# Kernel optimization log

Measured on AMD Instinct MI355X. Metric: run time of the kernel, lower is better.

## Reference

```python
import jax, jax.numpy as jnp
import numpy as np

B, C0, N, K = 8, 3, 2048, 20
EMB = 1024
NUM_CLASS = 40
EPS = 1e-5
SLOPE = 0.2


def setup_inputs() -> dict:
    key = jax.random.key(0)
    ks = jax.random.split(key, 16)
    rn = lambda k, s: jax.random.normal(k, s, jnp.float32) * 0.05
    inp = {
        'x': jax.random.normal(ks[0], (B, C0, N), jnp.float32),
        # 1x1 conv weights (out_ch, in_ch)
        'w1': rn(ks[1], (64, 6)),
        'w2': rn(ks[2], (64, 128)),
        'w3': rn(ks[3], (128, 128)),
        'w4': rn(ks[4], (256, 256)),
        'w5': rn(ks[5], (EMB, 512)),
        # linear layers
        'lw1': rn(ks[6], (512, 2 * EMB)),
        'lw2': rn(ks[7], (256, 512)),
        'lb2': jnp.zeros((256,), jnp.float32),
        'lw3': rn(ks[8], (NUM_CLASS, 256)),
        'lb3': jnp.zeros((NUM_CLASS,), jnp.float32),
    }
    # batchnorm affine params (bn1..bn7)
    for i, c in zip(range(1, 8), (64, 64, 128, 256, EMB, 512, 256)):
        inp['g%d' % i] = jnp.ones((c,), jnp.float32)
        inp['b%d' % i] = jnp.zeros((c,), jnp.float32)
    return inp


def lrelu(x):
    return jnp.where(x >= 0, x, SLOPE * x)


def bn(x, g, b, axes):
    # training-mode batchnorm over `axes`, channel axis = 1 (or last for 2D)
    m = jnp.mean(x, axis=axes, keepdims=True)
    v = jnp.var(x, axis=axes, keepdims=True)
    shp = [1] * x.ndim
    ch_ax = 1 if x.ndim > 1 else 0
    shp[ch_ax] = g.shape[0]
    return (x - m) * jax.lax.rsqrt(v + EPS) * g.reshape(shp) + b.reshape(shp)


def knn_idx(x, k):
    # x: [B, C, N]; topk of -||xi - xj||^2 -> k nearest (incl. self)
    inner = -2.0 * jnp.einsum('bcn,bcm->bnm', x, x)
    xx = jnp.sum(x * x, axis=1)  # [B, N]
    pd = -xx[:, :, None] - inner - xx[:, None, :]
    return jax.lax.top_k(pd, k)[1]  # [B, N, k]


def graph_feature(x, k):
    # x: [B, C, N] -> [B, 2C, N, k]
    b_, c_, n_ = x.shape
    idx = knn_idx(x, k)
    xt = jnp.transpose(x, (0, 2, 1))  # [B, N, C]
    nbr = xt[jnp.arange(b_)[:, None, None], idx]  # [B, N, k, C] irregular gather
    ctr = xt[:, :, None, :]
    feat = jnp.concatenate([nbr - ctr, jnp.broadcast_to(ctr, nbr.shape)], axis=-1)
    return jnp.transpose(feat, (0, 3, 1, 2))


def edge_block(x, w, g, b, k):
    f = graph_feature(x, k)                      # [B, 2C, N, k]
    y = jnp.einsum('oc,bcnk->bonk', w, f)        # 1x1 conv2d
    y = lrelu(bn(y, g, b, (0, 2, 3)))
    return jnp.max(y, axis=-1)                   # max over k -> [B, O, N]


def reference(x, w1, w2, w3, w4, w5, lw1, lw2, lb2, lw3, lb3,
              g1, b1, g2, b2, g3, b3, g4, b4, g5, b5, g6, b6, g7, b7):
    x1 = edge_block(x, w1, g1, b1, K)   # [B, 64, N]
    x2 = edge_block(x1, w2, g2, b2, K)  # [B, 64, N]
    x3 = edge_block(x2, w3, g3, b3, K)  # [B, 128, N]
    x4 = edge_block(x3, w4, g4, b4, K)  # [B, 256, N]
    cat = jnp.concatenate([x1, x2, x3, x4], axis=1)  # [B, 512, N]
    y = lrelu(bn(jnp.einsum('oc,bcn->bon', w5, cat), g5, b5, (0, 2)))  # [B, EMB, N]
    p = jnp.concatenate([jnp.max(y, axis=-1), jnp.mean(y, axis=-1)], axis=1)  # [B, 2*EMB]
    h = lrelu(bn(p @ lw1.T, g6, b6, (0,)))
    h = lrelu(bn(h @ lw2.T + lb2, g7, b7, (0,)))  # dropout = identity (eval)
    return h @ lw3.T + lb3  # [B, NUM_CLASS]
```

## Files before the change

kernel.cpp:

```cpp
#include <hip/hip_runtime.h>
#include <float.h>

constexpr int cB = 8;
constexpr int cN = 2048;
constexpr int cKnn = 20;
constexpr float F_EPS = 1e-5f;
constexpr float F_SLOPE = 0.2f;

__device__ __forceinline__ float lrelu(float x){ return x >= 0.f ? x : F_SLOPE * x; }

typedef __bf16 bf16x8 __attribute__((ext_vector_type(8)));
typedef float  f32x4  __attribute__((ext_vector_type(4)));
union U16x8 { uint4 u; bf16x8 v; };

__device__ __forceinline__ unsigned short f2bf(float x){
    unsigned u = __builtin_bit_cast(unsigned, x);
    unsigned r = u + 0x7FFFu + ((u >> 16) & 1u);
    return (unsigned short)(r >> 16);
}
__device__ __forceinline__ float bf2f(unsigned short h){
    return __builtin_bit_cast(float, (unsigned)h << 16);
}
__device__ __forceinline__ bf16x8 ldfrag(const unsigned short* p){
    U16x8 t; t.u = *(const uint4*)p; return t.v;
}

__global__ void k_transpose3(const float* __restrict__ x, float* __restrict__ xt, float* __restrict__ xx){
    int i = blockIdx.x * 256 + threadIdx.x;
    if(i >= cB * cN) return;
    int b = i / cN, n = i % cN;
    const float* xb = x + (size_t)b * 3 * cN;
    float a = xb[n], c = xb[cN + n], d = xb[2*cN + n];
    float* o = xt + (size_t)i * 4;
    o[0] = a; o[1] = c; o[2] = d; o[3] = 0.f;
    xx[i] = a*a + c*c + d*d;
}

template<int C>
__global__ void k_xx(const float* __restrict__ xt, float* __restrict__ xx){
    int i = blockIdx.x * 256 + threadIdx.x;
    if(i >= cB * cN) return;
    const float4* r4 = (const float4*)(xt + (size_t)i * C);
    float s = 0.f;
    #pragma unroll
    for(int c = 0; c < C/4; c++){
        float4 v = r4[c];
        s += v.x*v.x + v.y*v.y + v.z*v.z + v.w*v.w;
    }
    xx[i] = s;
}

template<int C>
__global__ void k_mkhl(const float* __restrict__ xt, unsigned short* __restrict__ xhl){
    int i = blockIdx.x * 256 + threadIdx.x;
    if(i >= cB * cN * C) return;
    int c = i % C; size_t bn = (size_t)i / C;
    float x = xt[bn * C + c];
    unsigned short h = f2bf(x);
    unsigned short l = f2bf(x - bf2f(h));
    xhl[bn * 2 * C + c] = h;
    xhl[bn * 2 * C + C + c] = l;
}

template<int C>
__global__ __launch_bounds__(256) void k_score(const float* __restrict__ xt, const float* __restrict__ xx,
                                               float* __restrict__ S, int b_base){
    __shared__ float at[16][68];
    __shared__ float bt[16][68];
    int tid = threadIdx.x;
    int j0 = blockIdx.x * 64, q0 = blockIdx.y * 64, z = blockIdx.z;
    int b = b_base + z;
    const float* Xb = xt + (size_t)b * cN * C;
    int no = tid % 16, mo = tid / 16;
    float acc[4][4] = {};
    {
        if(tid < 64){
            float4 v = *(const float4*)(Xb + (size_t)(q0 + tid) * C);
            at[0][tid] = v.x; at[1][tid] = v.y; at[2][tid] = v.z; at[3][tid] = v.w;
            float4 w = *(const float4*)(Xb + (size_t)(j0 + tid) * C);
            bt[0][tid] = w.x; bt[1][tid] = w.y; bt[2][tid] = w.z; bt[3][tid] = w.w;
        }
        __syncthreads();
        #pragma unroll
        for(int c = 0; c < C; c++){
            float av[4] = { at[c][mo*4+0], at[c][mo*4+1], at[c][mo*4+2], at[c][mo*4+3] };
            float bv[4] = { bt[c][no*4+0], bt[c][no*4+1], bt[c][no*4+2], bt[c][no*4+3] };
            #pragma unroll
            for(int i2 = 0; i2 < 4; i2++)
                #pragma unroll
                for(int j2 = 0; j2 < 4; j2++)
                    acc[i2][j2] += av[i2] * bv[j2];
        }
    }
    const float* xxb = xx + (size_t)b * cN;
    float4 xv = *(const float4*)(xxb + j0 + no * 4);
    #pragma unroll
    for(int i2 = 0; i2 < 4; i2++){
        float4 o = make_float4(2.f*acc[i2][0] - xv.x, 2.f*acc[i2][1] - xv.y,
                               2.f*acc[i2][2] - xv.z, 2.f*acc[i2][3] - xv.w);
        *(float4*)(S + ((size_t)z * cN + q0 + mo * 4 + i2) * cN + j0 + no * 4) = o;
    }
}

template<int C>
__global__ __launch_bounds__(256) void k_score_mfma(const unsigned short* __restrict__ XHL,
                                                    const float* __restrict__ xx,
                                                    float* __restrict__ S, int b_base){
    constexpr int SROW = 2 * C;
    constexpr int KST = C / 32;
    __shared__ unsigned short As[128 * 40];
    __shared__ unsigned short Bs[128 * 40];
    int tid = threadIdx.x;
    int lane = tid & 63, wave = tid >> 6;
    int wm = wave & 1, wn = wave >> 1;
    int q0 = blockIdx.y * 128, j0 = blockIdx.x * 128, z = blockIdx.z;
    int b = b_base + z;
    const unsigned short* Xb = XHL + (size_t)b * cN * SROW;
    int m = lane & 15, quad = lane >> 4;
    f32x4 acc[4][4] = {};

    for(int seg = 0; seg < 3; seg++){
        int aoff = (seg == 2) ? C : 0;
        int boff = (seg == 1) ? C : 0;
        for(int kk = 0; kk < KST; kk++){
            __syncthreads();
            #pragma unroll
            for(int h = 0; h < 2; h++){
                int cidx = tid + h * 256;
                int row = cidx >> 2, cc = cidx & 3;
                *(uint4*)&As[row*40 + cc*8] = *(const uint4*)(Xb + (size_t)(q0 + row) * SROW + aoff + kk*32 + cc*8);
                *(uint4*)&Bs[row*40 + cc*8] = *(const uint4*)(Xb + (size_t)(j0 + row) * SROW + boff + kk*32 + cc*8);
            }
            __syncthreads();
            bf16x8 af[4], bfr[4];
            #pragma unroll
            for(int t = 0; t < 4; t++){
                af[t]  = ldfrag(&As[(wm*64 + t*16 + m)*40 + quad*8]);
                bfr[t] = ldfrag(&Bs[(wn*64 + t*16 + m)*40 + quad*8]);
            }
            #pragma unroll
            for(int i = 0; i < 4; i++)
                #pragma unroll
                for(int j = 0; j < 4; j++)
                    acc[i][j] = __builtin_amdgcn_mfma_f32_16x16x32_bf16(af[i], bfr[j], acc[i][j], 0, 0, 0);
        }
    }
    const float* xxb = xx + (size_t)b * cN;
    #pragma unroll
    for(int j = 0; j < 4; j++){
        int jj = j0 + wn*64 + j*16 + m;
        float xv = xxb[jj];
        #pragma unroll
        for(int i = 0; i < 4; i++){
            int r0 = q0 + wm*64 + i*16 + quad*4;
            #pragma unroll
            for(int r = 0; r < 4; r++)
                S[((size_t)z * cN + r0 + r) * cN + jj] = 2.f * acc[i][j][r] - xv;
        }
    }
}

__global__ __launch_bounds__(256) void k_select(const float* __restrict__ S, int* __restrict__ idxout,
                                                int b_base){
    __shared__ unsigned skey[2][44];
    __shared__ int      sidx[2][44];
    int tid = threadIdx.x;
    int wave = tid >> 6, lane = tid & 63;
    int row = wave >> 1;
    int w   = wave & 1;
    int n = blockIdx.x * 2 + row;
    int z = blockIdx.y;
    const float* rowp = S + ((size_t)z * cN + n) * cN + w * 1024;
    unsigned key[16];
    #pragma unroll
    for(int i = 0; i < 16; i++){
        float s = rowp[i * 64 + lane];
        unsigned u = __float_as_uint(s);
        key[i] = (s >= 0.f) ? (u | 0x80000000u) : ~u;
    }
    unsigned T = 0; bool exact = false;
    for(int bit = 31; bit >= 0; bit--){
        unsigned test = T | (1u << bit);
        int c = 0;
        #pragma unroll
        for(int i = 0; i < 16; i++) c += (key[i] >= test) ? 1 : 0;
        #pragma unroll
        for(int off = 32; off; off >>= 1) c += __shfl_xor(c, off);
        if(c >= cKnn){
            T = test;
            if(c == cKnn){ exact = true; break; }
        }
    }
    int jbase = w * 1024;
    int pos = 0;
    if(exact){
        #pragma unroll
        for(int i = 0; i < 16; i++){
            bool hi = key[i] >= T;
            unsigned long long mm = __ballot(hi);
            if(hi){
                int r = __popcll(mm & ((1ull << lane) - 1ull));
                skey[row][w*20 + pos + r] = key[i];
                sidx[row][w*20 + pos + r] = jbase + i*64 + lane;
            }
            pos += __popcll(mm);
        }
    } else {
        int nab = 0;
        #pragma unroll
        for(int i = 0; i < 16; i++) nab += (key[i] > T) ? 1 : 0;
        #pragma unroll
        for(int off = 32; off; off >>= 1) nab += __shfl_xor(nab, off);
        int need = cKnn - nab;
        #pragma unroll
        for(int i = 0; i < 16; i++){
            bool hi = key[i] > T;
            unsigned long long mm = __ballot(hi);
            if(hi){
                int r = __popcll(mm & ((1ull << lane) - 1ull));
                skey[row][w*20 + pos + r] = key[i];
                sidx[row][w*20 + pos + r] = jbase + i*64 + lane;
            }
            pos += __popcll(mm);
        }
        for(int i = 0; i < 16 && need > 0; i++){
            bool eq = (key[i] == T);
            unsigned long long mm = __ballot(eq);
            int r = __popcll(mm & ((1ull << lane) - 1ull));
            if(eq && r < need){
                skey[row][w*20 + pos + r] = key[i];
                sidx[row][w*20 + pos + r] = jbase + i*64 + lane;
            }
            int t = __popcll(mm); t = t < need ? t : need;
            pos += t; need -= t;
        }
    }
    __syncthreads();
    if(w) return;
    unsigned k40 = (lane < 40) ? skey[row][lane] : 0u;
    int      j40 = (lane < 40) ? sidx[row][lane] : 0;
    unsigned Tg = 0; bool ex = false;
    for(int bit = 31; bit >= 0; bit--){
        unsigned test = Tg | (1u << bit);
        int c = __popcll(__ballot((lane < 40) && (k40 >= test)));
        if(c >= cKnn){
            Tg = test;
            if(c == cKnn){ ex = true; break; }
        }
    }
    int* out = idxout + ((size_t)(b_base + z) * cN + n) * cKnn;
    if(ex){
        bool hi = (lane < 40) && (k40 >= Tg);
        unsigned long long mm = __ballot(hi);
        if(hi){ int r = __popcll(mm & ((1ull << lane) - 1ull)); out[r] = j40; }
    } else {
        bool hi = (lane < 40) && (k40 > Tg);
        unsigned long long mm = __ballot(hi);
        if(hi){ int r = __popcll(mm & ((1ull << lane) - 1ull)); out[r] = j40; }
        int nab = __popcll(mm);
        int need = cKnn - nab;
        bool eq = (lane < 40) && (k40 == Tg);
        unsigned long long me = __ballot(eq);
        int r = __popcll(me & ((1ull << lane) - 1ull));
        if(eq && r < need) out[nab + r] = j40;
    }
}

template<int Cin, int O, int CP>
__global__ void k_prepww(const float* __restrict__ w, float* __restrict__ ww){
    int e = blockIdx.x * 256 + threadIdx.x;
    if(e >= CP * 2 * O) return;
    int op = e % (2 * O), c = e / (2 * O);
    float val = 0.f;
    if(c < Cin){
        if(op < O) val = w[op * 2 * Cin + c];
        else { int o = op - O; val = w[o * 2 * Cin + Cin + c] - w[o * 2 * Cin + c]; }
    }
    ww[c * 2 * O + op] = val;
}

template<int Cin, int O, int CP>
__global__ void k_prepww_split(const float* __restrict__ w, unsigned short* __restrict__ whl){
    int e = blockIdx.x * 256 + threadIdx.x;
    if(e >= 2 * O * CP) return;
    int c = e % CP, o2 = e / CP;
    float val = 0.f;
    if(c < Cin){
        if(o2 < O) val = w[o2 * 2 * Cin + c];
        else { int o = o2 - O; val = w[o * 2 * Cin + Cin + c] - w[o * 2 * Cin + c]; }
    }
    unsigned short h = f2bf(val);
    unsigned short l = f2bf(val - bf2f(h));
    whl[(size_t)o2 * 2 * CP + c] = h;
    whl[(size_t)o2 * 2 * CP + CP + c] = l;
}

template<int K, int W2O>
__global__ __launch_bounds__(256) void k_uw(const float* __restrict__ xt, const float* __restrict__ ww,
                                            float* __restrict__ UW){
    __shared__ float at[16][68];
    __shared__ float bt[16][68];
    int tid = threadIdx.x;
    int o0 = blockIdx.x * 64, q0 = blockIdx.y * 64, b = blockIdx.z;
    const float* Xb = xt + (size_t)b * cN * K;
    int no = tid % 16, mo = tid / 16;
    float acc[4][4] = {};
    {
        if(tid < 64){
            float4 v = *(const float4*)(Xb + (size_t)(q0 + tid) * K);
            at[0][tid] = v.x; at[1][tid] = v.y; at[2][tid] = v.z; at[3][tid] = v.w;
            int cc = tid >> 4, n4 = tid & 15;
            float4 wv = *(const float4*)(ww + (size_t)cc * W2O + o0 + n4 * 4);
            bt[cc][n4*4+0] = wv.x; bt[cc][n4*4+1] = wv.y;
            bt[cc][n4*4+2] = wv.z; bt[cc][n4*4+3] = wv.w;
        }
        __syncthreads();
        #pragma unroll
        for(int c = 0; c < K; c++){
            float av[4] = { at[c][mo*4+0], at[c][mo*4+1], at[c][mo*4+2], at[c][mo*4+3] };
            float bv[4] = { bt[c][no*4+0], bt[c][no*4+1], bt[c][no*4+2], bt[c][no*4+3] };
            #pragma unroll
            for(int i2 = 0; i2 < 4; i2++)
                #pragma unroll
                for(int j2 = 0; j2 < 4; j2++)
                    acc[i2][j2] += av[i2] * bv[j2];
        }
    }
    #pragma unroll
    for(int i2 = 0; i2 < 4; i2++){
        float4 v = make_float4(acc[i2][0], acc[i2][1], acc[i2][2], acc[i2][3]);
        *(float4*)(UW + ((size_t)b * cN + q0 + mo * 4 + i2) * W2O + o0 + no * 4) = v;
    }
}

template<int C, int W2O>
__global__ __launch_bounds__(256) void k_uw_mfma(const unsigned short* __restrict__ XHL,
                                                 const unsigned short* __restrict__ WHL,
                                                 float* __restrict__ UW){
    constexpr int SROW = 2 * C;
    constexpr int KST = C / 32;
    __shared__ unsigned short As[128 * 40];
    __shared__ unsigned short Bs[128 * 40];
    int tid = threadIdx.x;
    int lane = tid & 63, wave = tid >> 6;
    int wm = wave & 1, wn = wave >> 1;
    int n0 = blockIdx.x * 128, q0 = blockIdx.y * 128, b = blockIdx.z;
    const unsigned short* Xb = XHL + (size_t)b * cN * SROW;
    int m = lane & 15, quad = lane >> 4;
    f32x4 acc[4][4] = {};

    for(int seg = 0; seg < 3; seg++){
        int aoff = (seg == 2) ? C : 0;
        int boff = (seg == 1) ? C : 0;
        for(int kk = 0; kk < KST; kk++){
            __syncthreads();
            #pragma unroll
            for(int h = 0; h < 2; h++){
                int cidx = tid + h * 256;
                int row = cidx >> 2, cc = cidx & 3;
                *(uint4*)&As[row*40 + cc*8] = *(const uint4*)(Xb + (size_t)(q0 + row) * SROW + aoff + kk*32 + cc*8);
                *(uint4*)&Bs[row*40 + cc*8] = *(const uint4*)(WHL + (size_t)(n0 + row) * SROW + boff + kk*32 + cc*8);
            }
            __syncthreads();
            bf16x8 af[4], bfr[4];
            #pragma unroll
            for(int t = 0; t < 4; t++){
                af[t]  = ldfrag(&As[(wm*64 + t*16 + m)*40 + quad*8]);
                bfr[t] = ldfrag(&Bs[(wn*64 + t*16 + m)*40 + quad*8]);
            }
            #pragma unroll
            for(int i = 0; i < 4; i++)
                #pragma unroll
                for(int j = 0; j < 4; j++)
                    acc[i][j] = __builtin_amdgcn_mfma_f32_16x16x32_bf16(af[i], bfr[j], acc[i][j], 0, 0, 0);
        }
    }
    #pragma unroll
    for(int i = 0; i < 4; i++){
        int r0 = q0 + wm*64 + i*16 + quad*4;
        #pragma unroll
        for(int j = 0; j < 4; j++){
            int col = n0 + wn*64 + j*16 + m;
            #pragma unroll
            for(int r = 0; r < 4; r++)
                UW[((size_t)b * cN + r0 + r) * W2O + col] = acc[i][j][r];
        }
    }
}

template<int O>
__global__ __launch_bounds__(256) void k_gmax(const float* __restrict__ UW, const int* __restrict__ idx,
                                              float* __restrict__ Mbuf, float* __restrict__ bsum, float* __restrict__ bsq){
    constexpr int VEC = O / 64;
    constexpr int W2O = 2 * O;
    int id = blockIdx.x;
    int b = id & 7;
    int base = (id >> 3) * 16;
    int tid = threadIdx.x;
    int w = tid >> 6, l = tid & 63;
    const float* U = UW + (size_t)b * cN * W2O;
    float lsum[VEC] = {}, lsq[VEC] = {};
    for(int p = 0; p < 4; p++){
        int n = base + w * 4 + p;
        const int* ip = idx + ((size_t)b * cN + n) * cKnn;
        int jj[cKnn];
        #pragma unroll
        for(int k = 0; k < cKnn; k++) jj[k] = ip[k];
        float mx[VEC], su[VEC] = {}, s2[VEC] = {};
        #pragma unroll
        for(int v = 0; v < VEC; v++) mx[v] = -FLT_MAX;
        #pragma unroll
        for(int k = 0; k < cKnn; k++){
            const float* ur = U + (size_t)jj[k] * W2O + l * VEC;
            float uv[VEC];
            if constexpr (VEC == 4){ float4 t = *(const float4*)ur; uv[0]=t.x; uv[1]=t.y; uv[2]=t.z; uv[3]=t.w; }
            else if constexpr (VEC == 2){ float2 t = *(const float2*)ur; uv[0]=t.x; uv[1]=t.y; }
            else { uv[0] = *ur; }
            #pragma unroll
            for(int v = 0; v < VEC; v++){
                mx[v] = fmaxf(mx[v], uv[v]); su[v] += uv[v]; s2[v] += uv[v]*uv[v];
            }
        }
        const float* wr = U + (size_t)n * W2O + O + l * VEC;
        float w2[VEC];
        if constexpr (VEC == 4){ float4 t = *(const float4*)wr; w2[0]=t.x; w2[1]=t.y; w2[2]=t.z; w2[3]=t.w; }
        else if constexpr (VEC == 2){ float2 t = *(const float2*)wr; w2[0]=t.x; w2[1]=t.y; }
        else { w2[0] = *wr; }
        float* mp = Mbuf + ((size_t)b * cN + n) * O + l * VEC;
        if constexpr (VEC == 4){
            *(float4*)mp = make_float4(mx[0]+w2[0], mx[1]+w2[1], mx[2]+w2[2], mx[3]+w2[3]);
        } else if constexpr (VEC == 2){
            *(float2*)mp = make_float2(mx[0]+w2[0], mx[1]+w2[1]);
        } else {
            *mp = mx[0] + w2[0];
        }
        #pragma unroll
        for(int v = 0; v < VEC; v++){
            lsum[v] += su[v] + (float)cKnn * w2[v];
            lsq[v]  += s2[v] + 2.f * w2[v] * su[v] + (float)cKnn * w2[v] * w2[v];
        }
    }
    int bkt = id & 63;
    #pragma unroll
    for(int v = 0; v < VEC; v++){
        atomicAdd(&bsum[bkt * O + l * VEC + v], lsum[v]);
        atomicAdd(&bsq [bkt * O + l * VEC + v], lsq[v]);
    }
}

template<int O>
__global__ void k_redstats(const float* __restrict__ bsum, const float* __restrict__ bsq,
                           const float* __restrict__ g, const float* __restrict__ bb,
                           float2* __restrict__ stats, float invcnt){
    int o = threadIdx.x;
    if(o >= O) return;
    float s = 0.f, q = 0.f;
    for(int k = 0; k < 64; k++){ s += bsum[k * O + o]; q += bsq[k * O + o]; }
    float m = s * invcnt;
    float v = q * invcnt - m * m;
    float sc = g[o] * rsqrtf(v + F_EPS);
    stats[o] = make_float2(sc, bb[o] - m * sc);
}

template<int O, bool WXT>
__global__ void k_norm(const float* __restrict__ Mbuf, const float2* __restrict__ stats,
                       unsigned short* __restrict__ catb, float* __restrict__ xtn, int ooff){
    size_t i = (size_t)blockIdx.x * 256 + threadIdx.x;
    if(i >= (size_t)cB * cN * O) return;
    int o = i % O;
    size_t bn = i / O;
    float2 st = stats[o];
    float y = lrelu(Mbuf[i] * st.x + st.y);
    catb[bn * 512 + ooff + o] = f2bf(y);
    if(WXT) xtn[i] = y;
}

__global__ void k_cvtw5(const float* __restrict__ w5, unsigned short* __restrict__ w5b){
    int i = blockIdx.x * 256 + threadIdx.x;
    if(i >= 1024 * 512) return;
    w5b[i] = f2bf(w5[i]);
}

__global__ __launch_bounds__(256) void k_gemm_z_mfma(const unsigned short* __restrict__ W5B,
                                                     const unsigned short* __restrict__ CATB,
                                                     float* __restrict__ z){
    __shared__ unsigned short As[128 * 40];
    __shared__ unsigned short Bs[128 * 40];
    int tid = threadIdx.x;
    int lane = tid & 63, wave = tid >> 6;
    int wm = wave & 1, wn = wave >> 1;
    int n0 = blockIdx.x * 128, o0 = blockIdx.y * 128, b = blockIdx.z;
    const unsigned short* Cb = CATB + (size_t)b * cN * 512;
    int m = lane & 15, quad = lane >> 4;
    f32x4 acc[4][4] = {};

    for(int kk = 0; kk < 16; kk++){
        __syncthreads();
        #pragma unroll
        for(int h = 0; h < 2; h++){
            int cidx = tid + h * 256;
            int row = cidx >> 2, cc = cidx & 3;
            *(uint4*)&As[row*40 + cc*8] = *(const uint4*)(W5B + (size_t)(o0 + row) * 512 + kk*32 + cc*8);
            *(uint4*)&Bs[row*40 + cc*8] = *(const uint4*)(Cb  + (size_t)(n0 + row) * 512 + kk*32 + cc*8);
        }
        __syncthreads();
        bf16x8 af[4], bfr[4];
        #pragma unroll
        for(int t = 0; t < 4; t++){
            af[t]  = ldfrag(&As[(wm*64 + t*16 + m)*40 + quad*8]);
            bfr[t] = ldfrag(&Bs[(wn*64 + t*16 + m)*40 + quad*8]);
        }
        #pragma unroll
        for(int i = 0; i < 4; i++)
            #pragma unroll
            for(int j = 0; j < 4; j++)
                acc[i][j] = __builtin_amdgcn_mfma_f32_16x16x32_bf16(af[i], bfr[j], acc[i][j], 0, 0, 0);
    }
    #pragma unroll
    for(int i = 0; i < 4; i++){
        int r0 = o0 + wm*64 + i*16 + quad*4;
        #pragma unroll
        for(int j = 0; j < 4; j++){
            int col = n0 + wn*64 + j*16 + m;
            #pragma unroll
            for(int r = 0; r < 4; r++)
                z[((size_t)b * 1024 + r0 + r) * cN + col] = acc[i][j][r];
        }
    }
}

__global__ void k_zstats(const float* __restrict__ z, const float* __restrict__ g5,
                         const float* __restrict__ b5, float2* __restrict__ stats){
    int o = blockIdx.x;
    int tid = threadIdx.x;
    __shared__ float ss[256], sq[256];
    float s = 0.f, q = 0.f;
    for(int e = tid; e < cB * cN; e += 256){
        int b = e >> 11, n = e & 2047;
        float v = z[((size_t)b * 1024 + o) * cN + n];
        s += v; q += v * v;
    }
    ss[tid] = s; sq[tid] = q; __syncthreads();
    for(int st = 128; st; st >>= 1){
        if(tid < st){ ss[tid] += ss[tid + st]; sq[tid] += sq[tid + st]; }
        __syncthreads();
    }
    if(tid == 0){
        float m = ss[0] / (float)(cB * cN);
        float v = sq[0] / (float)(cB * cN) - m * m;
        float sc = g5[o] * rsqrtf(v + F_EPS);
        stats[o] = make_float2(sc, b5[o] - m * sc);
    }
}

__global__ void k_pool(const float* __restrict__ z, const float2* __restrict__ stats,
                       float* __restrict__ p){
    int o = blockIdx.x, b = blockIdx.y;
    int tid = threadIdx.x;
    float2 st = stats[o];
    const float* row = z + ((size_t)b * 1024 + o) * cN;
    float mx = -FLT_MAX, sm = 0.f;
    for(int n = tid; n < cN; n += 256){
        float y = lrelu(row[n] * st.x + st.y);
        mx = fmaxf(mx, y); sm += y;
    }
    __shared__ float smx[256], ssm[256];
    smx[tid] = mx; ssm[tid] = sm; __syncthreads();
    for(int st2 = 128; st2; st2 >>= 1){
        if(tid < st2){ smx[tid] = fmaxf(smx[tid], smx[tid + st2]); ssm[tid] += ssm[tid + st2]; }
        __syncthreads();
    }
    if(tid == 0){
        p[(size_t)b * 2048 + o] = smx[0];
        p[(size_t)b * 2048 + 1024 + o] = ssm[0] * (1.f / cN);
    }
}

__global__ void k_fc1(const float* __restrict__ p, const float* __restrict__ lw1,
                      const float* __restrict__ g6, const float* __restrict__ b6,
                      float* __restrict__ h1){
    int f = blockIdx.x;
    int tid = threadIdx.x;
    const float* wrow = lw1 + (size_t)f * 2048;
    float acc[cB] = {};
    for(int i = tid; i < 2048; i += 64){
        float wv = wrow[i];
        #pragma unroll
        for(int b = 0; b < cB; b++) acc[b] += p[(size_t)b * 2048 + i] * wv;
    }
    #pragma unroll
    for(int b = 0; b < cB; b++){
        float v = acc[b];
        for(int off = 32; off; off >>= 1) v += __shfl_down(v, off);
        acc[b] = v;
    }
    if(tid == 0){
        float m = 0.f;
        #pragma unroll
        for(int b = 0; b < cB; b++) m += acc[b];
        m *= (1.f / cB);
        float var = 0.f;
        #pragma unroll
        for(int b = 0; b < cB; b++){ float d = acc[b] - m; var += d * d; }
        var *= (1.f / cB);
        float sc = g6[f] * rsqrtf(var + F_EPS);
        float sh = b6[f] - m * sc;
        #pragma unroll
        for(int b = 0; b < cB; b++) h1[(size_t)b * 512 + f] = lrelu(acc[b] * sc + sh);
    }
}

__global__ void k_fc2(const float* __restrict__ h1, const float* __restrict__ lw2,
                      const float* __restrict__ lb2, const float* __restrict__ g7,
                      const float* __restrict__ b7, float* __restrict__ h2){
    int f = blockIdx.x;
    int tid = threadIdx.x;
    const float* wrow = lw2 + (size_t)f * 512;
    float acc[cB] = {};
    for(int i = tid; i < 512; i += 64){
        float wv = wrow[i];
        #pragma unroll
        for(int b = 0; b < cB; b++) acc[b] += h1[(size_t)b * 512 + i] * wv;
    }
    #pragma unroll
    for(int b = 0; b < cB; b++){
        float v = acc[b];
        for(int off = 32; off; off >>= 1) v += __shfl_down(v, off);
        acc[b] = v;
    }
    if(tid == 0){
        float bias = lb2[f];
        #pragma unroll
        for(int b = 0; b < cB; b++) acc[b] += bias;
        float m = 0.f;
        #pragma unroll
        for(int b = 0; b < cB; b++) m += acc[b];
        m *= (1.f / cB);
        float var = 0.f;
        #pragma unroll
        for(int b = 0; b < cB; b++){ float d = acc[b] - m; var += d * d; }
        var *= (1.f / cB);
        float sc = g7[f] * rsqrtf(var + F_EPS);
        float sh = b7[f] - m * sc;
        #pragma unroll
        for(int b = 0; b < cB; b++) h2[(size_t)b * 256 + f] = lrelu(acc[b] * sc + sh);
    }
}

__global__ void k_fc3(const float* __restrict__ h2, const float* __restrict__ lw3,
                      const float* __restrict__ lb3, float* __restrict__ out){
    int cls = blockIdx.x;
    int tid = threadIdx.x;
    const float* wrow = lw3 + (size_t)cls * 256;
    float acc[cB] = {};
    for(int i = tid; i < 256; i += 64){
        float wv = wrow[i];
        #pragma unroll
        for(int b = 0; b < cB; b++) acc[b] += h2[(size_t)b * 256 + i] * wv;
    }
    #pragma unroll
    for(int b = 0; b < cB; b++){
        float v = acc[b];
        for(int off = 32; off; off >>= 1) v += __shfl_down(v, off);
        acc[b] = v;
    }
    if(tid == 0){
        float bias = lb3[cls];
        #pragma unroll
        for(int b = 0; b < cB; b++) out[(size_t)b * 40 + cls] = acc[b] + bias;
    }
}

extern "C" void kernel_launch(void* const* d_in, const int* in_sizes, int n_in,
                              void* d_out, int out_size, void* d_ws, size_t ws_size,
                              hipStream_t stream){
    (void)in_sizes; (void)n_in; (void)out_size; (void)ws_size;
    const float* x   = (const float*)d_in[0];
    const float* w1  = (const float*)d_in[1];
    const float* w2  = (const float*)d_in[2];
    const float* w3  = (const float*)d_in[3];
    const float* w4  = (const float*)d_in[4];
    const float* w5  = (const float*)d_in[5];
    const float* lw1 = (const float*)d_in[6];
    const float* lw2 = (const float*)d_in[7];
    const float* lb2 = (const float*)d_in[8];
    const float* lw3 = (const float*)d_in[9];
    const float* lb3 = (const float*)d_in[10];
    const float* g1 = (const float*)d_in[11]; const float* b1 = (const float*)d_in[12];
    const float* g2 = (const float*)d_in[13]; const float* b2 = (const float*)d_in[14];
    const float* g3 = (const float*)d_in[15]; const float* b3 = (const float*)d_in[16];
    const float* g4 = (const float*)d_in[17]; const float* b4 = (const float*)d_in[18];
    const float* g5 = (const float*)d_in[19]; const float* b5 = (const float*)d_in[20];
    const float* g6 = (const float*)d_in[21]; const float* b6 = (const float*)d_in[22];
    const float* g7 = (const float*)d_in[23]; const float* b7 = (const float*)d_in[24];

    char* base = (char*)d_ws;
    size_t off = 0;
    auto alloc = [&](size_t bytes) -> char* {
        char* pp = base + off;
        off += (bytes + 255) & ~(size_t)255;
        return pp;
    };
    float*  XT   = (float*) alloc(sizeof(float) * (size_t)cB * cN * 128);
    float*  Z    = (float*) alloc(sizeof(float) * (size_t)cB * 1024 * cN);
    float*  MB   = (float*) alloc(sizeof(float) * (size_t)cB * cN * 256);
    int*    IDX  = (int*)   alloc(sizeof(int)   * (size_t)cB * cN * cKnn);
    float*  XX   = (float*) alloc(sizeof(float) * (size_t)cB * cN);
    float*  BSUM = (float*) alloc(sizeof(float) * 64 * 256);
    float*  BSQ  = (float*) alloc(sizeof(float) * 64 * 256);
    float2* STATS= (float2*)alloc(sizeof(float2) * 1024);
    float*  WW   = (float*) alloc(sizeof(float) * 4 * 128);
    unsigned short* WHL  = (unsigned short*)alloc(sizeof(short) * 512 * 256);
    unsigned short* XHL  = (unsigned short*)alloc(sizeof(short) * (size_t)cB * cN * 256);
    unsigned short* CATB = (unsigned short*)alloc(sizeof(short) * (size_t)cB * cN * 512);
    unsigned short* W5B  = (unsigned short*)alloc(sizeof(short) * 1024 * 512);
    float*  P    = (float*) alloc(sizeof(float) * (size_t)cB * 2048);
    float*  H1   = (float*) alloc(sizeof(float) * (size_t)cB * 512);
    float*  H2   = (float*) alloc(sizeof(float) * (size_t)cB * 256);
    float*  SC   = Z;
    float*  UW   = Z;

    const float invcnt = 1.f / (float)(cB * cN * cKnn);
    dim3 sc1Grid(cN / 64, cN / 64, 4);
    dim3 scmGrid(cN / 128, cN / 128, 4);
    dim3 selGrid(cN / 2, 4);
    int gmBlocks = (cN / 16) * cB;

    k_transpose3<<<64, 256, 0, stream>>>(x, XT, XX);
    for(int h = 0; h < 2; h++){
        k_score<4><<<sc1Grid, 256, 0, stream>>>(XT, XX, SC, 4 * h);
        k_select<<<selGrid, 256, 0, stream>>>(SC, IDX, 4 * h);
    }
    k_prepww<3, 64, 4><<<2, 256, 0, stream>>>(w1, WW);
    hipMemsetAsync(BSUM, 0, sizeof(float) * 2 * 64 * 256, stream);
    k_uw<4, 128><<<dim3(2, 32, cB), 256, 0, stream>>>(XT, WW, UW);
    k_gmax<64><<<gmBlocks, 256, 0, stream>>>(UW, IDX, MB, BSUM, BSQ);
    k_redstats<64><<<1, 256, 0, stream>>>(BSUM, BSQ, g1, b1, STATS, invcnt);
    k_norm<64, true><<<(cB * cN * 64) / 256, 256, 0, stream>>>(MB, STATS, CATB, XT, 0);

    k_xx<64><<<64, 256, 0, stream>>>(XT, XX);
    k_mkhl<64><<<(cB * cN * 64) / 256, 256, 0, stream>>>(XT, XHL);
    for(int h = 0; h < 2; h++){
        k_score_mfma<64><<<scmGrid, 256, 0, stream>>>(XHL, XX, SC, 4 * h);
        k_select<<<selGrid, 256, 0, stream>>>(SC, IDX, 4 * h);
    }
    k_prepww_split<64, 64, 64><<<(128 * 64) / 256, 256, 0, stream>>>(w2, WHL);
    hipMemsetAsync(BSUM, 0, sizeof(float) * 2 * 64 * 256, stream);
    k_uw_mfma<64, 128><<<dim3(1, 16, cB), 256, 0, stream>>>(XHL, WHL, UW);
    k_gmax<64><<<gmBlocks, 256, 0, stream>>>(UW, IDX, MB, BSUM, BSQ);
    k_redstats<64><<<1, 256, 0, stream>>>(BSUM, BSQ, g2, b2, STATS, invcnt);
    k_norm<64, true><<<(cB * cN * 64) / 256, 256, 0, stream>>>(MB, STATS, CATB, XT, 64);

    k_xx<64><<<64, 256, 0, stream>>>(XT, XX);
    k_mkhl<64><<<(cB * cN * 64) / 256, 256, 0, stream>>>(XT, XHL);
    for(int h = 0; h < 2; h++){
        k_score_mfma<64><<<scmGrid, 256, 0, stream>>>(XHL, XX, SC, 4 * h);
        k_select<<<selGrid, 256, 0, stream>>>(SC, IDX, 4 * h);
    }
    k_prepww_split<64, 128, 64><<<(256 * 64) / 256, 256, 0, stream>>>(w3, WHL);
    hipMemsetAsync(BSUM, 0, sizeof(float) * 2 * 64 * 256, stream);
    k_uw_mfma<64, 256><<<dim3(2, 16, cB), 256, 0, stream>>>(XHL, WHL, UW);
    k_gmax<128><<<gmBlocks, 256, 0, stream>>>(UW, IDX, MB, BSUM, BSQ);
    k_redstats<128><<<1, 256, 0, stream>>>(BSUM, BSQ, g3, b3, STATS, invcnt);
    k_norm<128, true><<<(cB * cN * 128) / 256, 256, 0, stream>>>(MB, STATS, CATB, XT, 128);

    k_xx<128><<<64, 256, 0, stream>>>(XT, XX);
    k_mkhl<128><<<(cB * cN * 128) / 256, 256, 0, stream>>>(XT, XHL);
    for(int h = 0; h < 2; h++){
        k_score_mfma<128><<<scmGrid, 256, 0, stream>>>(XHL, XX, SC, 4 * h);
        k_select<<<selGrid, 256, 0, stream>>>(SC, IDX, 4 * h);
    }
    k_prepww_split<128, 256, 128><<<(512 * 128) / 256, 256, 0, stream>>>(w4, WHL);
    hipMemsetAsync(BSUM, 0, sizeof(float) * 2 * 64 * 256, stream);
    k_uw_mfma<128, 512><<<dim3(4, 16, cB), 256, 0, stream>>>(XHL, WHL, UW);
    k_gmax<256><<<gmBlocks, 256, 0, stream>>>(UW, IDX, MB, BSUM, BSQ);
    k_redstats<256><<<1, 256, 0, stream>>>(BSUM, BSQ, g4, b4, STATS, invcnt);
    k_norm<256, false><<<(cB * cN * 256) / 256, 256, 0, stream>>>(MB, STATS, CATB, nullptr, 256);

    k_cvtw5<<<(1024 * 512) / 256, 256, 0, stream>>>(w5, W5B);
    k_gemm_z_mfma<<<dim3(cN / 128, 1024 / 128, cB), 256, 0, stream>>>(W5B, CATB, Z);
    k_zstats<<<1024, 256, 0, stream>>>(Z, g5, b5, STATS);
    k_pool<<<dim3(1024, cB), 256, 0, stream>>>(Z, STATS, P);
    k_fc1<<<512, 64, 0, stream>>>(P, lw1, g6, b6, H1);
    k_fc2<<<256, 64, 0, stream>>>(H1, lw2, lb2, g7, b7, H2);
    k_fc3<<<40, 64, 0, stream>>>(H2, lw3, lb3, (float*)d_out);
}
```

Measured before the change: 856.0 us.

## Fuse norm with bf16 split and squared-norm; batch all weight prep into one kernel

The batchnorm-apply kernel now writes the hi/lo bf16 split features and per-point squared norms directly, using wave shuffles and a small shared reduction. This removes the separate fp32 feature write, the k_xx and k_mkhl launches and their re-reads. All weight preprocessing (w1 through w5) is merged into one kernel launched up front, and the four stat-buffer memsets become a single memset over separate per-layer buffers. This cuts the launch count and memory traffic, at the cost of relying on the thread layout matching the channel counts O=64 and O=128 for the reductions.

```diff
diff --git a/kernel.cpp b/kernel.cpp
--- a/kernel.cpp
+++ b/kernel.cpp
@@ -36,30 +36,45 @@
     xx[i] = a*a + c*c + d*d;
 }
 
-template<int C>
-__global__ void k_xx(const float* __restrict__ xt, float* __restrict__ xx){
-    int i = blockIdx.x * 256 + threadIdx.x;
-    if(i >= cB * cN) return;
-    const float4* r4 = (const float4*)(xt + (size_t)i * C);
-    float s = 0.f;
-    #pragma unroll
-    for(int c = 0; c < C/4; c++){
-        float4 v = r4[c];
-        s += v.x*v.x + v.y*v.y + v.z*v.z + v.w*v.w;
-    }
-    xx[i] = s;
-}
-
-template<int C>
-__global__ void k_mkhl(const float* __restrict__ xt, unsigned short* __restrict__ xhl){
-    int i = blockIdx.x * 256 + threadIdx.x;
-    if(i >= cB * cN * C) return;
-    int c = i % C; size_t bn = (size_t)i / C;
-    float x = xt[bn * C + c];
-    unsigned short h = f2bf(x);
-    unsigned short l = f2bf(x - bf2f(h));
-    xhl[bn * 2 * C + c] = h;
-    xhl[bn * 2 * C + C + c] = l;
+template<int Cin, int O, int CP>
+__device__ __forceinline__ void prep_split_elem(const float* __restrict__ w, unsigned short* __restrict__ whl, int e){
+    int c = e % CP, o2 = e / CP;
+    float val = 0.f;
+    if(c < Cin){
+        if(o2 < O) val = w[o2 * 2 * Cin + c];
+        else { int o = o2 - O; val = w[o * 2 * Cin + Cin + c] - w[o * 2 * Cin + c]; }
+    }
+    unsigned short h = f2bf(val);
+    unsigned short l = f2bf(val - bf2f(h));
+    whl[(size_t)o2 * 2 * CP + c] = h;
+    whl[(size_t)o2 * 2 * CP + CP + c] = l;
+}
+
+__global__ void k_prepall(const float* __restrict__ w1, const float* __restrict__ w2,
+                          const float* __restrict__ w3, const float* __restrict__ w4,
+                          const float* __restrict__ w5,
+                          float* __restrict__ ww, unsigned short* __restrict__ whl2,
+                          unsigned short* __restrict__ whl3, unsigned short* __restrict__ whl4,
+                          unsigned short* __restrict__ w5b){
+    int e = blockIdx.x * 256 + threadIdx.x;
+    if(e < 512){
+        int op = e % 128, c = e / 128;
+        float val = 0.f;
+        if(c < 3){
+            if(op < 64) val = w1[op * 6 + c];
+            else { int o = op - 64; val = w1[o * 6 + 3 + c] - w1[o * 6 + c]; }
+        }
+        ww[e] = val;
+        return;
+    }
+    e -= 512;
+    if(e < 8192){ prep_split_elem<64, 64, 64>(w2, whl2, e); return; }
+    e -= 8192;
+    if(e < 16384){ prep_split_elem<64, 128, 64>(w3, whl3, e); return; }
+    e -= 16384;
+    if(e < 65536){ prep_split_elem<128, 256, 128>(w4, whl4, e); return; }
+    e -= 65536;
+    if(e < 524288) w5b[e] = f2bf(w5[e]);
 }
 
 template<int C>
@@ -266,35 +281,6 @@
     }
 }
 
-template<int Cin, int O, int CP>
-__global__ void k_prepww(const float* __restrict__ w, float* __restrict__ ww){
-    int e = blockIdx.x * 256 + threadIdx.x;
-    if(e >= CP * 2 * O) return;
-    int op = e % (2 * O), c = e / (2 * O);
-    float val = 0.f;
-    if(c < Cin){
-        if(op < O) val = w[op * 2 * Cin + c];
-        else { int o = op - O; val = w[o * 2 * Cin + Cin + c] - w[o * 2 * Cin + c]; }
-    }
-    ww[c * 2 * O + op] = val;
-}
-
-template<int Cin, int O, int CP>
-__global__ void k_prepww_split(const float* __restrict__ w, unsigned short* __restrict__ whl){
-    int e = blockIdx.x * 256 + threadIdx.x;
-    if(e >= 2 * O * CP) return;
-    int c = e % CP, o2 = e / CP;
-    float val = 0.f;
-    if(c < Cin){
-        if(o2 < O) val = w[o2 * 2 * Cin + c];
-        else { int o = o2 - O; val = w[o * 2 * Cin + Cin + c] - w[o * 2 * Cin + c]; }
-    }
-    unsigned short h = f2bf(val);
-    unsigned short l = f2bf(val - bf2f(h));
-    whl[(size_t)o2 * 2 * CP + c] = h;
-    whl[(size_t)o2 * 2 * CP + CP + c] = l;
-}
-
 template<int K, int W2O>
 __global__ __launch_bounds__(256) void k_uw(const float* __restrict__ xt, const float* __restrict__ ww,
                                             float* __restrict__ UW){
@@ -463,22 +449,34 @@
 }
 
 template<int O, bool WXT>
-__global__ void k_norm(const float* __restrict__ Mbuf, const float2* __restrict__ stats,
-                       unsigned short* __restrict__ catb, float* __restrict__ xtn, int ooff){
-    size_t i = (size_t)blockIdx.x * 256 + threadIdx.x;
-    if(i >= (size_t)cB * cN * O) return;
+__global__ void k_normf(const float* __restrict__ Mbuf, const float2* __restrict__ stats,
+                        unsigned short* __restrict__ catb, unsigned short* __restrict__ xhl,
+                        float* __restrict__ xx, int ooff){
+    __shared__ float part[4];
+    int tid = threadIdx.x;
+    size_t i = (size_t)blockIdx.x * 256 + tid;
     int o = i % O;
     size_t bn = i / O;
     float2 st = stats[o];
     float y = lrelu(Mbuf[i] * st.x + st.y);
     catb[bn * 512 + ooff + o] = f2bf(y);
-    if(WXT) xtn[i] = y;
-}
-
-__global__ void k_cvtw5(const float* __restrict__ w5, unsigned short* __restrict__ w5b){
-    int i = blockIdx.x * 256 + threadIdx.x;
-    if(i >= 1024 * 512) return;
-    w5b[i] = f2bf(w5[i]);
+    if constexpr (WXT){
+        unsigned short h = f2bf(y);
+        unsigned short l = f2bf(y - bf2f(h));
+        xhl[bn * 2 * O + o] = h;
+        xhl[bn * 2 * O + O + o] = l;
+        float s = y * y;
+        #pragma unroll
+        for(int off = 32; off; off >>= 1) s += __shfl_xor(s, off);
+        if constexpr (O == 64){
+            if((tid & 63) == 0) xx[bn] = s;
+        } else {
+            int wv = tid >> 6;
+            if((tid & 63) == 0) part[wv] = s;
+            __syncthreads();
+            if((tid & 127) == 0) xx[bn] = part[wv] + part[wv + 1];
+        }
+    }
 }
 
 __global__ __launch_bounds__(256) void k_gemm_z_mfma(const unsigned short* __restrict__ W5B,
@@ -701,16 +699,17 @@
         off += (bytes + 255) & ~(size_t)255;
         return pp;
     };
-    float*  XT   = (float*) alloc(sizeof(float) * (size_t)cB * cN * 128);
+    float*  XT   = (float*) alloc(sizeof(float) * (size_t)cB * cN * 4);
     float*  Z    = (float*) alloc(sizeof(float) * (size_t)cB * 1024 * cN);
     float*  MB   = (float*) alloc(sizeof(float) * (size_t)cB * cN * 256);
     int*    IDX  = (int*)   alloc(sizeof(int)   * (size_t)cB * cN * cKnn);
     float*  XX   = (float*) alloc(sizeof(float) * (size_t)cB * cN);
-    float*  BSUM = (float*) alloc(sizeof(float) * 64 * 256);
-    float*  BSQ  = (float*) alloc(sizeof(float) * 64 * 256);
+    float*  BS   = (float*) alloc(sizeof(float) * 4 * 2 * 64 * 256);
     float2* STATS= (float2*)alloc(sizeof(float2) * 1024);
     float*  WW   = (float*) alloc(sizeof(float) * 4 * 128);
-    unsigned short* WHL  = (unsigned short*)alloc(sizeof(short) * 512 * 256);
+    unsigned short* WHL2 = (unsigned short*)alloc(sizeof(short) * 128 * 128);
+    unsigned short* WHL3 = (unsigned short*)alloc(sizeof(short) * 256 * 128);
+    unsigned short* WHL4 = (unsigned short*)alloc(sizeof(short) * 512 * 256);
     unsigned short* XHL  = (unsigned short*)alloc(sizeof(short) * (size_t)cB * cN * 256);
     unsigned short* CATB = (unsigned short*)alloc(sizeof(short) * (size_t)cB * cN * 512);
     unsigned short* W5B  = (unsigned short*)alloc(sizeof(short) * 1024 * 512);
@@ -719,6 +718,10 @@
     float*  H2   = (float*) alloc(sizeof(float) * (size_t)cB * 256);
     float*  SC   = Z;
     float*  UW   = Z;
+    float* BSUM0 = BS + 0 * 2 * 16384, *BSQ0 = BSUM0 + 16384;
+    float* BSUM1 = BS + 1 * 2 * 16384, *BSQ1 = BSUM1 + 16384;
+    float* BSUM2 = BS + 2 * 2 * 16384, *BSQ2 = BSUM2 + 16384;
+    float* BSUM3 = BS + 3 * 2 * 16384, *BSQ3 = BSUM3 + 16384;
 
     const float invcnt = 1.f / (float)(cB * cN * cKnn);
     dim3 sc1Grid(cN / 64, cN / 64, 4);
@@ -727,57 +730,45 @@
     int gmBlocks = (cN / 16) * cB;
 
     k_transpose3<<<64, 256, 0, stream>>>(x, XT, XX);
+    k_prepall<<<(614912 + 255) / 256, 256, 0, stream>>>(w1, w2, w3, w4, w5, WW, WHL2, WHL3, WHL4, W5B);
+    hipMemsetAsync(BS, 0, sizeof(float) * 4 * 2 * 16384, stream);
+
     for(int h = 0; h < 2; h++){
         k_score<4><<<sc1Grid, 256, 0, stream>>>(XT, XX, SC, 4 * h);
         k_select<<<selGrid, 256, 0, stream>>>(SC, IDX, 4 * h);
     }
-    k_prepww<3, 64, 4><<<2, 256, 0, stream>>>(w1, WW);
-    hipMemsetAsync(BSUM, 0, sizeof(float) * 2 * 64 * 256, stream);
     k_uw<4, 128><<<dim3(2, 32, cB), 256, 0, stream>>>(XT, WW, UW);
-    k_gmax<64><<<gmBlocks, 256, 0, stream>>>(UW, IDX, MB, BSUM, BSQ);
-    k_redstats<64><<<1, 256, 0, stream>>>(BSUM, BSQ, g1, b1, STATS, invcnt);
-    k_norm<64, true><<<(cB * cN * 64) / 256, 256, 0, stream>>>(MB, STATS, CATB, XT, 0);
-
-    k_xx<64><<<64, 256, 0, stream>>>(XT, XX);
-    k_mkhl<64><<<(cB * cN * 64) / 256, 256, 0, stream>>>(XT, XHL);
+    k_gmax<64><<<gmBlocks, 256, 0, stream>>>(UW, IDX, MB, BSUM0, BSQ0);
+    k_redstats<64><<<1, 256, 0, stream>>>(BSUM0, BSQ0, g1, b1, STATS, invcnt);
+    k_normf<64, true><<<(cB * cN * 64) / 256, 256, 0, stream>>>(MB, STATS, CATB, XHL, XX, 0);
+
     for(int h = 0; h < 2; h++){
         k_score_mfma<64><<<scmGrid, 256, 0, stream>>>(XHL, XX, SC, 4 * h);
         k_select<<<selGrid, 256, 0, stream>>>(SC, IDX, 4 * h);
     }
-    k_prepww_split<64, 64, 64><<<(128 * 64) / 256, 256, 0, stream>>>(w2, WHL);
-    hipMemsetAsync(BSUM, 0, sizeof(float) * 2 * 64 * 256, stream);
-    k_uw_mfma<64, 128><<<dim3(1, 16, cB), 256, 0, stream>>>(XHL, WHL, UW);
-    k_gmax<64><<<gmBlocks, 256, 0, stream>>>(UW, IDX, MB, BSUM, BSQ);
-    k_redstats<64><<<1, 256, 0, stream>>>(BSUM, BSQ, g2, b2, STATS, invcnt);
-    k_norm<64, true><<<(cB * cN * 64) / 256, 256, 0, stream>>>(MB, STATS, CATB, XT, 64);
-
-    k_xx<64><<<64, 256, 0, stream>>>(XT, XX);
-    k_mkhl<64><<<(cB * cN * 64) / 256, 256, 0, stream>>>(XT, XHL);
+    k_uw_mfma<64, 128><<<dim3(1, 16, cB), 256, 0, stream>>>(XHL, WHL2, UW);
+    k_gmax<64><<<gmBlocks, 256, 0, stream>>>(UW, IDX, MB, BSUM1, BSQ1);
+    k_redstats<64><<<1, 256, 0, stream>>>(BSUM1, BSQ1, g2, b2, STATS, invcnt);
+    k_normf<64, true><<<(cB * cN * 64) / 256, 256, 0, stream>>>(MB, STATS, CATB, XHL, XX, 64);
+
     for(int h = 0; h < 2; h++){
         k_score_mfma<64><<<scmGrid, 256, 0, stream>>>(XHL, XX, SC, 4 * h);
         k_select<<<selGrid, 256, 0, stream>>>(SC, IDX, 4 * h);
     }
-    k_prepww_split<64, 128, 64><<<(256 * 64) / 256, 256, 0, stream>>>(w3, WHL);
-    hipMemsetAsync(BSUM, 0, sizeof(float) * 2 * 64 * 256, stream);
-    k_uw_mfma<64, 256><<<dim3(2, 16, cB), 256, 0, stream>>>(XHL, WHL, UW);
-    k_gmax<128><<<gmBlocks, 256, 0, stream>>>(UW, IDX, MB, BSUM, BSQ);
-    k_redstats<128><<<1, 256, 0, stream>>>(BSUM, BSQ, g3, b3, STATS, invcnt);
-    k_norm<128, true><<<(cB * cN * 128) / 256, 256, 0, stream>>>(MB, STATS, CATB, XT, 128);
-
-    k_xx<128><<<64, 256, 0, stream>>>(XT, XX);
-    k_mkhl<128><<<(cB * cN * 128) / 256, 256, 0, stream>>>(XT, XHL);
+    k_uw_mfma<64, 256><<<dim3(2, 16, cB), 256, 0, stream>>>(XHL, WHL3, UW);
+    k_gmax<128><<<gmBlocks, 256, 0, stream>>>(UW, IDX, MB, BSUM2, BSQ2);
+    k_redstats<128><<<1, 256, 0, stream>>>(BSUM2, BSQ2, g3, b3, STATS, invcnt);
+    k_normf<128, true><<<(cB * cN * 128) / 256, 256, 0, stream>>>(MB, STATS, CATB, XHL, XX, 128);
+
     for(int h = 0; h < 2; h++){
         k_score_mfma<128><<<scmGrid, 256, 0, stream>>>(XHL, XX, SC, 4 * h);
         k_select<<<selGrid, 256, 0, stream>>>(SC, IDX, 4 * h);
     }
-    k_prepww_split<128, 256, 128><<<(512 * 128) / 256, 256, 0, stream>>>(w4, WHL);
-    hipMemsetAsync(BSUM, 0, sizeof(float) * 2 * 64 * 256, stream);
-    k_uw_mfma<128, 512><<<dim3(4, 16, cB), 256, 0, stream>>>(XHL, WHL, UW);
-    k_gmax<256><<<gmBlocks, 256, 0, stream>>>(UW, IDX, MB, BSUM, BSQ);
-    k_redstats<256><<<1, 256, 0, stream>>>(BSUM, BSQ, g4, b4, STATS, invcnt);
-    k_norm<256, false><<<(cB * cN * 256) / 256, 256, 0, stream>>>(MB, STATS, CATB, nullptr, 256);
-
-    k_cvtw5<<<(1024 * 512) / 256, 256, 0, stream>>>(w5, W5B);
+    k_uw_mfma<128, 512><<<dim3(4, 16, cB), 256, 0, stream>>>(XHL, WHL4, UW);
+    k_gmax<256><<<gmBlocks, 256, 0, stream>>>(UW, IDX, MB, BSUM3, BSQ3);
+    k_redstats<256><<<1, 256, 0, stream>>>(BSUM3, BSQ3, g4, b4, STATS, invcnt);
+    k_normf<256, false><<<(cB * cN * 256) / 256, 256, 0, stream>>>(MB, STATS, CATB, nullptr, nullptr, 256);
+
     k_gemm_z_mfma<<<dim3(cN / 128, 1024 / 128, cB), 256, 0, stream>>>(W5B, CATB, Z);
     k_zstats<<<1024, 256, 0, stream>>>(Z, g5, b5, STATS);
     k_pool<<<dim3(1024, cB), 256, 0, stream>>>(Z, STATS, P);
```

Measured after the change: 823.7 us. -3.8%, faster.
